# Kernel optimization log

Hardware: AMD Instinct MI355X
Metric: run time of the kernel (lower is better)

## Reference

```python
import jax, jax.numpy as jnp
import numpy as np

N_NODES = 50000
IN_CH, HID_CH, OUT_CH = 128, 128, 64
N_EDGES = 800000


def setup_inputs() -> dict:
    key = jax.random.key(0)
    k = jax.random.split(key, 6)
    x = jax.random.normal(k[0], (N_NODES, IN_CH), dtype=jnp.float32)
    edge_index = jax.random.randint(k[1], (2, N_EDGES), 0, N_NODES, dtype=jnp.int64)
    # Glorot-ish init for weights
    W1 = jax.random.normal(k[2], (IN_CH, HID_CH), dtype=jnp.float32) * (1.0 / np.sqrt(IN_CH))
    b1 = jnp.zeros((HID_CH,), dtype=jnp.float32)
    W2 = jax.random.normal(k[3], (HID_CH, OUT_CH), dtype=jnp.float32) * (1.0 / np.sqrt(HID_CH))
    b2 = jnp.zeros((OUT_CH,), dtype=jnp.float32)
    return {"x": x, "edge_index": edge_index, "W1": W1, "b1": b1, "W2": W2, "b2": b2}


def _gcn_conv(x, src, dst, W, b, n_nodes):
    """PyG GCNConv: linear, add self-loops, symmetric deg^-1/2 normalization, scatter-add."""
    h = x @ W  # [N, F_out]
    loop = jnp.arange(n_nodes, dtype=src.dtype)
    s = jnp.concatenate([src, loop])  # [E+N]
    d = jnp.concatenate([dst, loop])
    # in-degree on target nodes (including self-loops), edge weight = 1
    deg = jnp.zeros((n_nodes,), dtype=h.dtype).at[d].add(1.0)
    dinv = jnp.where(deg > 0, jax.lax.rsqrt(deg), 0.0)
    norm = dinv[s] * dinv[d]  # [E+N]
    msg = h[s] * norm[:, None]  # [E+N, F_out]
    out = jax.ops.segment_sum(msg, d, num_segments=n_nodes)
    return out + b


def reference(x, edge_index, W1, b1, W2, b2):
    src, dst = edge_index[0], edge_index[1]
    h = _gcn_conv(x, src, dst, W1, b1, N_NODES)
    h = jax.nn.relu(h)
    # dropout in eval mode -> identity
    out = _gcn_conv(h, src, dst, W2, b2, N_NODES)
    return out
```

## Files before the change

### kernel.cpp

```cpp
#include <hip/hip_runtime.h>

typedef __attribute__((ext_vector_type(8))) short bf16x8;
typedef __attribute__((ext_vector_type(4))) float f32x4;

constexpr int NN = 50000;
constexpr int NE = 800000;
constexpr int C1 = 128;
constexpr int C2 = 64;
constexpr int NBK = 196;
constexpr int EPB = 2048;
constexpr int NBLK = (NE + EPB - 1) / EPB;
constexpr int MT = NN / 16;
constexpr int MMB = 250;
constexpr int MMWAVES = MMB * 4;
constexpr int CAP = 8192;

__device__ __forceinline__ unsigned short f2bf(float f) {
    unsigned int u = __float_as_uint(f);
    u += 0x7FFFu + ((u >> 16) & 1u);
    return (unsigned short)(u >> 16);
}
__device__ __forceinline__ float2 bf2f(unsigned int u) {
    return make_float2(__uint_as_float(u << 16), __uint_as_float(u & 0xFFFF0000u));
}
__device__ __forceinline__ bf16x8 pack8(float4 a, float4 b) {
    bf16x8 r;
    r[0] = (short)f2bf(a.x); r[1] = (short)f2bf(a.y);
    r[2] = (short)f2bf(a.z); r[3] = (short)f2bf(a.w);
    r[4] = (short)f2bf(b.x); r[5] = (short)f2bf(b.y);
    r[6] = (short)f2bf(b.z); r[7] = (short)f2bf(b.w);
    return r;
}
__device__ __forceinline__ void addrow(float* a, uint4 v) {
    float2 p;
    p = bf2f(v.x); a[0] += p.x; a[1] += p.y;
    p = bf2f(v.y); a[2] += p.x; a[3] += p.y;
    p = bf2f(v.z); a[4] += p.x; a[5] += p.y;
    p = bf2f(v.w); a[6] += p.x; a[7] += p.y;
}

__global__ __launch_bounds__(256) void bin_kernel(const int* __restrict__ src,
                                                  const int* __restrict__ dst,
                                                  unsigned int* __restrict__ ebuf,
                                                  int* __restrict__ localOff) {
    __shared__ int lhist[NBK];
    __shared__ int ls[256];
    __shared__ int lcur[NBK];
    __shared__ unsigned int lbuf[EPB];
    const int t = threadIdx.x;
    const int base = blockIdx.x * EPB;
    if (t < NBK) lhist[t] = 0;
    __syncthreads();
    int b[8]; unsigned int p[8];
    #pragma unroll
    for (int i = 0; i < 8; i++) {
        int e = base + i * 256 + t;
        if (e < NE) {
            int s = src[e], d = dst[e];
            b[i] = d >> 8;
            p[i] = ((unsigned int)(d & 255) << 16) | (unsigned int)s;
            atomicAdd(&lhist[b[i]], 1);
        } else b[i] = -1;
    }
    __syncthreads();
    int v = (t < NBK) ? lhist[t] : 0;
    ls[t] = v;
    __syncthreads();
    #pragma unroll
    for (int d = 1; d < 256; d <<= 1) {
        int u = (t >= d) ? ls[t - d] : 0;
        __syncthreads();
        ls[t] += u;
        __syncthreads();
    }
    if (t < NBK) {
        lcur[t] = ls[t] - v;
        localOff[blockIdx.x * 200 + t] = ls[t] - v;
    }
    if (t == NBK - 1) localOff[blockIdx.x * 200 + NBK] = ls[t];
    __syncthreads();
    #pragma unroll
    for (int i = 0; i < 8; i++) {
        if (b[i] >= 0) {
            int lp = atomicAdd(&lcur[b[i]], 1);
            lbuf[lp] = p[i];
        }
    }
    __syncthreads();
    #pragma unroll
    for (int i = 0; i < 8; i++)
        ebuf[base + i * 256 + t] = lbuf[i * 256 + t];
}

__global__ __launch_bounds__(256) void place_kernel(const unsigned int* __restrict__ ebuf,
                                                    const int* __restrict__ localOff,
                                                    unsigned short* __restrict__ esrc,
                                                    int* __restrict__ cnt,
                                                    int* __restrict__ off,
                                                    float* __restrict__ dinv) {
    __shared__ unsigned int lbuf[CAP];
    __shared__ int lhist[256];
    __shared__ int ls[256];
    __shared__ int lcur[256];
    __shared__ int red[256];
    const int t = threadIdx.x;
    const int bkt = blockIdx.x;
    const int node0 = bkt << 8;
    const int nnodes = min(256, NN - node0);

    const int j0 = 2 * t, j1 = 2 * t + 1;
    int s0 = 0, l0 = 0, s1 = 0, l1 = 0;
    if (j0 < NBLK) { s0 = localOff[j0 * 200 + bkt]; l0 = localOff[j0 * 200 + bkt + 1] - s0; }
    if (j1 < NBLK) { s1 = localOff[j1 * 200 + bkt]; l1 = localOff[j1 * 200 + bkt + 1] - s1; }

    red[t] = s0 + s1;
    ls[t] = l0 + l1;
    lhist[t] = 0;
    __syncthreads();
    #pragma unroll
    for (int d = 1; d < 256; d <<= 1) {
        int u = (t >= d) ? ls[t - d] : 0;
        int r = (t + d < 256) ? red[t + d] : 0;
        __syncthreads();
        ls[t] += u;
        red[t] += r;
        __syncthreads();
    }
    const int segBase = red[0];
    const int total = ls[255];
    const int base0 = ls[t] - (l0 + l1);
    const int base1 = base0 + l0;
    const bool fits = (total <= CAP);

    if (fits) {
        const unsigned int* q0 = ebuf + j0 * EPB + s0;
        for (int k = 0; k < l0; k++) lbuf[base0 + k] = q0[k];
        const unsigned int* q1 = ebuf + j1 * EPB + s1;
        for (int k = 0; k < l1; k++) lbuf[base1 + k] = q1[k];
        __syncthreads();
        for (int k = t; k < total; k += 256) atomicAdd(&lhist[lbuf[k] >> 16], 1);
    } else {
        const unsigned int* q0 = ebuf + j0 * EPB + s0;
        for (int k = 0; k < l0; k++) atomicAdd(&lhist[q0[k] >> 16], 1);
        const unsigned int* q1 = ebuf + j1 * EPB + s1;
        for (int k = 0; k < l1; k++) atomicAdd(&lhist[q1[k] >> 16], 1);
    }
    __syncthreads();
    int v = lhist[t];
    ls[t] = v;
    __syncthreads();
    #pragma unroll
    for (int d = 1; d < 256; d <<= 1) {
        int u = (t >= d) ? ls[t - d] : 0;
        __syncthreads();
        ls[t] += u;
        __syncthreads();
    }
    int ex = ls[t] - v;
    lcur[t] = ex;
    if (t < nnodes) {
        cnt[node0 + t] = v;
        off[node0 + t] = segBase + ex;
        dinv[node0 + t] = rsqrtf((float)v + 1.0f);
    }
    __syncthreads();
    if (fits) {
        for (int k = t; k < total; k += 256) {
            unsigned int pp = lbuf[k];
            int lp = atomicAdd(&lcur[pp >> 16], 1);
            esrc[segBase + lp] = (unsigned short)(pp & 0xFFFFu);
        }
    } else {
        const unsigned int* q0 = ebuf + j0 * EPB + s0;
        for (int k = 0; k < l0; k++) {
            unsigned int pp = q0[k];
            int lp = atomicAdd(&lcur[pp >> 16], 1);
            esrc[segBase + lp] = (unsigned short)(pp & 0xFFFFu);
        }
        const unsigned int* q1 = ebuf + j1 * EPB + s1;
        for (int k = 0; k < l1; k++) {
            unsigned int pp = q1[k];
            int lp = atomicAdd(&lcur[pp >> 16], 1);
            esrc[segBase + lp] = (unsigned short)(pp & 0xFFFFu);
        }
    }
}

__global__ __launch_bounds__(256, 2) void mm1_kernel(const float* __restrict__ x,
                                                     const float* __restrict__ W,
                                                     const float* __restrict__ dinv,
                                                     unsigned short* __restrict__ g1) {
    __shared__ unsigned short wl[4][8][64][8];
    const int t = threadIdx.x;
    for (int i = 0; i < 64; i++) {
        int idx = i * 256 + t;
        int k = idx >> 7, n = idx & 127;
        wl[k >> 5][n >> 4][((k >> 3) & 3) * 16 + (n & 15)][k & 7] = f2bf(W[idx]);
    }
    __syncthreads();
    const int lane = t & 63, lm = lane & 15, quad = lane >> 4;

    bf16x8 bfr[4][8];
    #pragma unroll
    for (int s = 0; s < 4; s++)
        #pragma unroll
        for (int nt = 0; nt < 8; nt++)
            bfr[s][nt] = *(const bf16x8*)&wl[s][nt][lane][0];

    int wg = blockIdx.x * 4 + (t >> 6);
    for (int tile = wg; tile < MT; tile += MMWAVES) {
        int row0 = tile << 4;
        const float* xr = x + (size_t)(row0 + lm) * 128 + quad * 8;
        bf16x8 af[4];
        #pragma unroll
        for (int s = 0; s < 4; s++) {
            float4 p = *(const float4*)(xr + s * 32);
            float4 q = *(const float4*)(xr + s * 32 + 4);
            af[s] = pack8(p, q);
        }
        f32x4 acc[8];
        #pragma unroll
        for (int nt = 0; nt < 8; nt++) acc[nt] = (f32x4){0.f, 0.f, 0.f, 0.f};
        #pragma unroll
        for (int s = 0; s < 4; s++)
            #pragma unroll
            for (int nt = 0; nt < 8; nt++)
                acc[nt] = __builtin_amdgcn_mfma_f32_16x16x32_bf16(af[s], bfr[s][nt],
                                                                  acc[nt], 0, 0, 0);
        float4 dv = *(const float4*)(dinv + row0 + quad * 4);
        float dvv[4] = {dv.x, dv.y, dv.z, dv.w};
        #pragma unroll
        for (int nt = 0; nt < 8; nt++)
            #pragma unroll
            for (int r = 0; r < 4; r++)
                g1[(size_t)(row0 + quad * 4 + r) * 128 + nt * 16 + lm] =
                    f2bf(acc[nt][r] * dvv[r]);
    }
}

__global__ __launch_bounds__(256, 2) void mm2_kernel(const unsigned short* __restrict__ x2,
                                                     const float* __restrict__ W,
                                                     const float* __restrict__ dinv,
                                                     unsigned short* __restrict__ g2) {
    __shared__ unsigned short wl[4][4][64][8];
    const int t = threadIdx.x;
    for (int i = 0; i < 32; i++) {
        int idx = i * 256 + t;
        int k = idx >> 6, n = idx & 63;
        wl[k >> 5][n >> 4][((k >> 3) & 3) * 16 + (n & 15)][k & 7] = f2bf(W[idx]);
    }
    __syncthreads();
    const int lane = t & 63, lm = lane & 15, quad = lane >> 4;

    bf16x8 bfr[4][4];
    #pragma unroll
    for (int s = 0; s < 4; s++)
        #pragma unroll
        for (int nt = 0; nt < 4; nt++)
            bfr[s][nt] = *(const bf16x8*)&wl[s][nt][lane][0];

    int wg = blockIdx.x * 4 + (t >> 6);
    for (int tile = wg; tile < MT; tile += MMWAVES) {
        int row0 = tile << 4;
        const bf16x8* xr = (const bf16x8*)(x2 + (size_t)(row0 + lm) * 128 + quad * 8);
        bf16x8 af[4];
        #pragma unroll
        for (int s = 0; s < 4; s++) af[s] = xr[s * 4];
        f32x4 acc[4];
        #pragma unroll
        for (int nt = 0; nt < 4; nt++) acc[nt] = (f32x4){0.f, 0.f, 0.f, 0.f};
        #pragma unroll
        for (int s = 0; s < 4; s++)
            #pragma unroll
            for (int nt = 0; nt < 4; nt++)
                acc[nt] = __builtin_amdgcn_mfma_f32_16x16x32_bf16(af[s], bfr[s][nt],
                                                                  acc[nt], 0, 0, 0);
        float4 dv = *(const float4*)(dinv + row0 + quad * 4);
        float dvv[4] = {dv.x, dv.y, dv.z, dv.w};
        #pragma unroll
        for (int nt = 0; nt < 4; nt++)
            #pragma unroll
            for (int r = 0; r < 4; r++)
                g2[(size_t)(row0 + quad * 4 + r) * 64 + nt * 16 + lm] =
                    f2bf(acc[nt][r] * dvv[r]);
    }
}

__global__ __launch_bounds__(256) void gather1_kernel(const unsigned short* __restrict__ g1,
                                                      const unsigned short* __restrict__ esrc,
                                                      const int* __restrict__ off,
                                                      const int* __restrict__ cnt,
                                                      const float* __restrict__ dinv,
                                                      const float* __restrict__ b1,
                                                      unsigned short* __restrict__ x2) {
    const int wave = threadIdx.x >> 6, lane = threadIdx.x & 63;
    const int slot = lane >> 4, part = lane & 15;
    int n = blockIdx.x * 4 + wave;
    if (n >= NN) return;
    const uint4* G = (const uint4*)g1;
    float a0[8] = {0,0,0,0,0,0,0,0};
    float a1[8] = {0,0,0,0,0,0,0,0};
    float a2[8] = {0,0,0,0,0,0,0,0};
    float a3[8] = {0,0,0,0,0,0,0,0};
    if (slot == 0) addrow(a0, G[(size_t)n * 16 + part]);
    int s0 = off[n], c = cnt[n];
    int i = slot;
    for (; i + 12 < c; i += 16) {
        int sA = esrc[s0 + i];
        int sB = esrc[s0 + i + 4];
        int sC = esrc[s0 + i + 8];
        int sD = esrc[s0 + i + 12];
        uint4 vA = G[(size_t)sA * 16 + part];
        uint4 vB = G[(size_t)sB * 16 + part];
        uint4 vC = G[(size_t)sC * 16 + part];
        uint4 vD = G[(size_t)sD * 16 + part];
        addrow(a0, vA);
        addrow(a1, vB);
        addrow(a2, vC);
        addrow(a3, vD);
    }
    for (; i < c; i += 4) addrow(a0, G[(size_t)esrc[s0 + i] * 16 + part]);
    #pragma unroll
    for (int j = 0; j < 8; j++) a0[j] += a1[j] + a2[j] + a3[j];
    #pragma unroll
    for (int j = 0; j < 8; j++) {
        a0[j] += __shfl_xor(a0[j], 16);
        a0[j] += __shfl_xor(a0[j], 32);
    }
    if (slot == 0) {
        float s = dinv[n];
        float4 bA = ((const float4*)b1)[part * 2];
        float4 bB = ((const float4*)b1)[part * 2 + 1];
        float4 p = make_float4(fmaxf(s * a0[0] + bA.x, 0.f), fmaxf(s * a0[1] + bA.y, 0.f),
                               fmaxf(s * a0[2] + bA.z, 0.f), fmaxf(s * a0[3] + bA.w, 0.f));
        float4 q = make_float4(fmaxf(s * a0[4] + bB.x, 0.f), fmaxf(s * a0[5] + bB.y, 0.f),
                               fmaxf(s * a0[6] + bB.z, 0.f), fmaxf(s * a0[7] + bB.w, 0.f));
        *(bf16x8*)(x2 + (size_t)n * 128 + part * 8) = pack8(p, q);
    }
}

__global__ __launch_bounds__(256) void gather2_kernel(const unsigned short* __restrict__ g2,
                                                      const unsigned short* __restrict__ esrc,
                                                      const int* __restrict__ off,
                                                      const int* __restrict__ cnt,
                                                      const float* __restrict__ dinv,
                                                      const float* __restrict__ b2,
                                                      float* __restrict__ out) {
    const int wave = threadIdx.x >> 6, lane = threadIdx.x & 63;
    const int slot = lane >> 3, part = lane & 7;
    int n = blockIdx.x * 4 + wave;
    if (n >= NN) return;
    const uint4* G = (const uint4*)g2;
    float a0[8] = {0,0,0,0,0,0,0,0};
    float a1[8] = {0,0,0,0,0,0,0,0};
    if (slot == 0) addrow(a0, G[(size_t)n * 8 + part]);
    int s0 = off[n], c = cnt[n];
    int i = slot;
    for (; i + 8 < c; i += 16) {
        int sA = esrc[s0 + i];
        int sB = esrc[s0 + i + 8];
        uint4 vA = G[(size_t)sA * 8 + part];
        uint4 vB = G[(size_t)sB * 8 + part];
        addrow(a0, vA);
        addrow(a1, vB);
    }
    if (i < c) addrow(a0, G[(size_t)esrc[s0 + i] * 8 + part]);
    #pragma unroll
    for (int j = 0; j < 8; j++) a0[j] += a1[j];
    #pragma unroll
    for (int j = 0; j < 8; j++) {
        a0[j] += __shfl_xor(a0[j], 8);
        a0[j] += __shfl_xor(a0[j], 16);
        a0[j] += __shfl_xor(a0[j], 32);
    }
    if (slot == 0) {
        float s = dinv[n];
        float4 bA = ((const float4*)b2)[part * 2];
        float4 bB = ((const float4*)b2)[part * 2 + 1];
        float* o = out + (size_t)n * 64 + part * 8;
        *(float4*)o = make_float4(s * a0[0] + bA.x, s * a0[1] + bA.y,
                                  s * a0[2] + bA.z, s * a0[3] + bA.w);
        *(float4*)(o + 4) = make_float4(s * a0[4] + bB.x, s * a0[5] + bB.y,
                                        s * a0[6] + bB.z, s * a0[7] + bB.w);
    }
}

extern "C" void kernel_launch(void* const* d_in, const int* in_sizes, int n_in,
                              void* d_out, int out_size, void* d_ws, size_t ws_size,
                              hipStream_t stream) {
    const float* x  = (const float*)d_in[0];
    const int* edges = (const int*)d_in[1];
    const float* W1 = (const float*)d_in[2];
    const float* b1 = (const float*)d_in[3];
    const float* W2 = (const float*)d_in[4];
    const float* b2 = (const float*)d_in[5];
    const int* src = edges;
    const int* dst = edges + NE;

    int* localOff  = (int*)d_ws;
    unsigned int* ebuf = (unsigned int*)(localOff + 78208);
    unsigned short* esrc = (unsigned short*)(ebuf + (size_t)NBLK * EPB);
    int* cnt       = (int*)(esrc + 800768);
    int* off       = cnt + 50048;
    float* dinv    = (float*)(off + 50048);
    unsigned short* g1 = (unsigned short*)(dinv + 50048);
    unsigned short* x2 = g1 + (size_t)NN * C1;
    unsigned short* g2 = g1;
    float* out = (float*)d_out;

    bin_kernel<<<NBLK, 256, 0, stream>>>(src, dst, ebuf, localOff);
    place_kernel<<<NBK, 256, 0, stream>>>(ebuf, localOff, esrc, cnt, off, dinv);

    mm1_kernel<<<MMB, 256, 0, stream>>>(x, W1, dinv, g1);
    gather1_kernel<<<(NN + 3) / 4, 256, 0, stream>>>(g1, esrc, off, cnt, dinv, b1, x2);

    mm2_kernel<<<MMB, 256, 0, stream>>>(x2, W2, dinv, g2);
    gather2_kernel<<<(NN + 3) / 4, 256, 0, stream>>>(g2, esrc, off, cnt, dinv, b2, out);
}
```

Baseline: 189.3 us.

## Split gather kernels across feature column slices with more edge-parallel lanes

Each gather wave now covers only a 4-lane column slice of a node's feature row (64 or 32 bytes) and uses 16 edge slots instead of 4 or 8. Blocks are indexed so that neighbouring blocks handle different slices of the same node group, which is meant to raise memory-level parallelism on nodes with few edges. The price is 4x (gather1) or 2x (gather2) more waves, repeated esrc/off/cnt reads per slice, narrower per-row accesses, extra shuffle-reduction steps, and no more loop unrolling.

```diff
diff --git a/kernel.cpp b/kernel.cpp
--- a/kernel.cpp
+++ b/kernel.cpp
@@ -293,49 +293,36 @@
                                                       const float* __restrict__ dinv,
                                                       const float* __restrict__ b1,
                                                       unsigned short* __restrict__ x2) {
-    const int wave = threadIdx.x >> 6, lane = threadIdx.x & 63;
-    const int slot = lane >> 4, part = lane & 15;
-    int n = blockIdx.x * 4 + wave;
-    if (n >= NN) return;
+    const int b = blockIdx.x;
+    const int slice = (b & 7) >> 1;
+    const int n = ((b >> 3) << 3) + ((b & 1) << 2) + (threadIdx.x >> 6);
+    const int lane = threadIdx.x & 63;
+    const int slot = lane >> 2, part = lane & 3;
+    const int col = slice * 4 + part;
     const uint4* G = (const uint4*)g1;
-    float a0[8] = {0,0,0,0,0,0,0,0};
-    float a1[8] = {0,0,0,0,0,0,0,0};
-    float a2[8] = {0,0,0,0,0,0,0,0};
-    float a3[8] = {0,0,0,0,0,0,0,0};
-    if (slot == 0) addrow(a0, G[(size_t)n * 16 + part]);
+    float a[8] = {0,0,0,0,0,0,0,0};
+    if (slot == 0) addrow(a, G[(size_t)n * 16 + col]);
     int s0 = off[n], c = cnt[n];
-    int i = slot;
-    for (; i + 12 < c; i += 16) {
-        int sA = esrc[s0 + i];
-        int sB = esrc[s0 + i + 4];
-        int sC = esrc[s0 + i + 8];
-        int sD = esrc[s0 + i + 12];
-        uint4 vA = G[(size_t)sA * 16 + part];
-        uint4 vB = G[(size_t)sB * 16 + part];
-        uint4 vC = G[(size_t)sC * 16 + part];
-        uint4 vD = G[(size_t)sD * 16 + part];
-        addrow(a0, vA);
-        addrow(a1, vB);
-        addrow(a2, vC);
-        addrow(a3, vD);
-    }
-    for (; i < c; i += 4) addrow(a0, G[(size_t)esrc[s0 + i] * 16 + part]);
-    #pragma unroll
-    for (int j = 0; j < 8; j++) a0[j] += a1[j] + a2[j] + a3[j];
+    for (int i = slot; i < c; i += 16) {
+        int s = esrc[s0 + i];
+        addrow(a, G[(size_t)s * 16 + col]);
+    }
     #pragma unroll
     for (int j = 0; j < 8; j++) {
-        a0[j] += __shfl_xor(a0[j], 16);
-        a0[j] += __shfl_xor(a0[j], 32);
+        a[j] += __shfl_xor(a[j], 4);
+        a[j] += __shfl_xor(a[j], 8);
+        a[j] += __shfl_xor(a[j], 16);
+        a[j] += __shfl_xor(a[j], 32);
     }
     if (slot == 0) {
-        float s = dinv[n];
-        float4 bA = ((const float4*)b1)[part * 2];
-        float4 bB = ((const float4*)b1)[part * 2 + 1];
-        float4 p = make_float4(fmaxf(s * a0[0] + bA.x, 0.f), fmaxf(s * a0[1] + bA.y, 0.f),
-                               fmaxf(s * a0[2] + bA.z, 0.f), fmaxf(s * a0[3] + bA.w, 0.f));
-        float4 q = make_float4(fmaxf(s * a0[4] + bB.x, 0.f), fmaxf(s * a0[5] + bB.y, 0.f),
-                               fmaxf(s * a0[6] + bB.z, 0.f), fmaxf(s * a0[7] + bB.w, 0.f));
-        *(bf16x8*)(x2 + (size_t)n * 128 + part * 8) = pack8(p, q);
+        float sc = dinv[n];
+        float4 bA = ((const float4*)b1)[col * 2];
+        float4 bB = ((const float4*)b1)[col * 2 + 1];
+        float4 p = make_float4(fmaxf(sc * a[0] + bA.x, 0.f), fmaxf(sc * a[1] + bA.y, 0.f),
+                               fmaxf(sc * a[2] + bA.z, 0.f), fmaxf(sc * a[3] + bA.w, 0.f));
+        float4 q = make_float4(fmaxf(sc * a[4] + bB.x, 0.f), fmaxf(sc * a[5] + bB.y, 0.f),
+                               fmaxf(sc * a[6] + bB.z, 0.f), fmaxf(sc * a[7] + bB.w, 0.f));
+        *(bf16x8*)(x2 + (size_t)n * 128 + col * 8) = pack8(p, q);
     }
 }
 
@@ -346,42 +333,36 @@
                                                       const float* __restrict__ dinv,
                                                       const float* __restrict__ b2,
                                                       float* __restrict__ out) {
-    const int wave = threadIdx.x >> 6, lane = threadIdx.x & 63;
-    const int slot = lane >> 3, part = lane & 7;
-    int n = blockIdx.x * 4 + wave;
-    if (n >= NN) return;
+    const int b = blockIdx.x;
+    const int slice = (b & 7) >> 2;
+    const int n = ((b >> 3) << 4) + ((b & 3) << 2) + (threadIdx.x >> 6);
+    const int lane = threadIdx.x & 63;
+    const int slot = lane >> 2, part = lane & 3;
+    const int col = slice * 4 + part;
     const uint4* G = (const uint4*)g2;
-    float a0[8] = {0,0,0,0,0,0,0,0};
-    float a1[8] = {0,0,0,0,0,0,0,0};
-    if (slot == 0) addrow(a0, G[(size_t)n * 8 + part]);
+    float a[8] = {0,0,0,0,0,0,0,0};
+    if (slot == 0) addrow(a, G[(size_t)n * 8 + col]);
     int s0 = off[n], c = cnt[n];
-    int i = slot;
-    for (; i + 8 < c; i += 16) {
-        int sA = esrc[s0 + i];
-        int sB = esrc[s0 + i + 8];
-        uint4 vA = G[(size_t)sA * 8 + part];
-        uint4 vB = G[(size_t)sB * 8 + part];
-        addrow(a0, vA);
-        addrow(a1, vB);
-    }
-    if (i < c) addrow(a0, G[(size_t)esrc[s0 + i] * 8 + part]);
-    #pragma unroll
-    for (int j = 0; j < 8; j++) a0[j] += a1[j];
+    for (int i = slot; i < c; i += 16) {
+        int s = esrc[s0 + i];
+        addrow(a, G[(size_t)s * 8 + col]);
+    }
     #pragma unroll
     for (int j = 0; j < 8; j++) {
-        a0[j] += __shfl_xor(a0[j], 8);
-        a0[j] += __shfl_xor(a0[j], 16);
-        a0[j] += __shfl_xor(a0[j], 32);
+        a[j] += __shfl_xor(a[j], 4);
+        a[j] += __shfl_xor(a[j], 8);
+        a[j] += __shfl_xor(a[j], 16);
+        a[j] += __shfl_xor(a[j], 32);
     }
     if (slot == 0) {
-        float s = dinv[n];
-        float4 bA = ((const float4*)b2)[part * 2];
-        float4 bB = ((const float4*)b2)[part * 2 + 1];
-        float* o = out + (size_t)n * 64 + part * 8;
-        *(float4*)o = make_float4(s * a0[0] + bA.x, s * a0[1] + bA.y,
-                                  s * a0[2] + bA.z, s * a0[3] + bA.w);
-        *(float4*)(o + 4) = make_float4(s * a0[4] + bB.x, s * a0[5] + bB.y,
-                                        s * a0[6] + bB.z, s * a0[7] + bB.w);
+        float sc = dinv[n];
+        float4 bA = ((const float4*)b2)[col * 2];
+        float4 bB = ((const float4*)b2)[col * 2 + 1];
+        float* o = out + (size_t)n * 64 + col * 8;
+        *(float4*)o = make_float4(sc * a[0] + bA.x, sc * a[1] + bA.y,
+                                  sc * a[2] + bA.z, sc * a[3] + bA.w);
+        *(float4*)(o + 4) = make_float4(sc * a[4] + bB.x, sc * a[5] + bB.y,
+                                        sc * a[6] + bB.z, sc * a[7] + bB.w);
     }
 }
 
@@ -412,8 +393,8 @@
     place_kernel<<<NBK, 256, 0, stream>>>(ebuf, localOff, esrc, cnt, off, dinv);
 
     mm1_kernel<<<MMB, 256, 0, stream>>>(x, W1, dinv, g1);
-    gather1_kernel<<<(NN + 3) / 4, 256, 0, stream>>>(g1, esrc, off, cnt, dinv, b1, x2);
+    gather1_kernel<<<NN, 256, 0, stream>>>(g1, esrc, off, cnt, dinv, b1, x2);
 
     mm2_kernel<<<MMB, 256, 0, stream>>>(x2, W2, dinv, g2);
-    gather2_kernel<<<(NN + 3) / 4, 256, 0, stream>>>(g2, esrc, off, cnt, dinv, b2, out);
-}
+    gather2_kernel<<<NN / 2, 256, 0, stream>>>(g2, esrc, off, cnt, dinv, b2, out);
+}
```

Result: slower. 251.2 us (+32.7%).
